# Kernel optimization log

Hardware: AMD Instinct MI355X
Metric: run time of the kernel (lower is better)

The kernel has to match this reference:

```python
import jax, jax.numpy as jnp
import numpy as np

EMBED_DIM = 512
NUM_HEADS = 8
HEAD_DIM = EMBED_DIM // NUM_HEADS
B, N, M = 4, 4096, 4096


def setup_inputs() -> dict:
    key = jax.random.key(0)
    ks = jax.random.split(key, 16)
    s = 0.02
    inp = {
        "query": jax.random.normal(ks[0], (B, N, EMBED_DIM), jnp.float32),
        "key": jax.random.normal(ks[1], (B, M, EMBED_DIM), jnp.float32),
        "value": jax.random.normal(ks[2], (B, M, EMBED_DIM), jnp.float32),
        # Linear weights stored as (in, out) so y = x @ W + b (== torch x @ W.T + b)
        "Wq": jax.random.normal(ks[3], (EMBED_DIM, EMBED_DIM), jnp.float32) * s,
        "bq": jnp.zeros((EMBED_DIM,), jnp.float32),
        "Wk": jax.random.normal(ks[4], (EMBED_DIM, EMBED_DIM), jnp.float32) * s,
        "bk": jnp.zeros((EMBED_DIM,), jnp.float32),
        "Wv": jax.random.normal(ks[5], (EMBED_DIM, EMBED_DIM), jnp.float32) * s,
        "bv": jnp.zeros((EMBED_DIM,), jnp.float32),
        # rank expansion MLP acts per-head on head_dim
        "W1": jax.random.normal(ks[6], (HEAD_DIM, HEAD_DIM * 2), jnp.float32) * s,
        "b1": jnp.zeros((HEAD_DIM * 2,), jnp.float32),
        "W2": jax.random.normal(ks[7], (HEAD_DIM * 2, HEAD_DIM), jnp.float32) * s,
        "b2": jnp.zeros((HEAD_DIM,), jnp.float32),
        "Wo": jax.random.normal(ks[8], (EMBED_DIM, EMBED_DIM), jnp.float32) * s,
        "bo": jnp.zeros((EMBED_DIM,), jnp.float32),
    }
    return inp


def reference(query, key, value, Wq, bq, Wk, bk, Wv, bv, W1, b1, W2, b2, Wo, bo):
    b, n, _ = query.shape
    m = key.shape[1]
    H, D = NUM_HEADS, HEAD_DIM
    # ELU+1 feature maps on projected q, k
    q = jax.nn.elu(query @ Wq + bq) + 1.0           # [B,N,E]
    k = jax.nn.elu(key @ Wk + bk) + 1.0             # [B,M,E]
    v = value @ Wv + bv                              # [B,M,E]
    q = q.reshape(b, n, H, D)
    k = k.reshape(b, m, H, D)
    v = v.reshape(b, m, H, D)
    # rank expansion MLP on keys (per head_dim), exact GELU as nn.GELU default
    k_aug = jax.nn.gelu(k @ W1 + b1, approximate=False) @ W2 + b2
    k_aug = jax.nn.elu(k_aug) + 1.0                  # [B,M,H,D]
    # inputs already fp32 (torch .float() casts are identity here)
    k_scaled = k_aug / m                             # normalize over context len
    kv_context = jnp.einsum('bmhd,bmhe->bhde', k_scaled, v)   # [B,H,D,D]
    out = jnp.einsum('bnhd,bhde->bnhe', q, kv_context)        # [B,N,H,D]
    k_sum = k_scaled.sum(axis=1)                      # [B,H,D]
    denom = jnp.einsum('bnhd,bhd->bnh', q, k_sum)     # [B,N,H]
    out = out / jnp.clip(denom, 1e-6, None)[..., None]
    out = jnp.clip(jnp.nan_to_num(out, nan=0.0, posinf=65000.0, neginf=-65000.0),
                   -65000.0, 65000.0)
    out = out.reshape(b, n, H * D)
    return out @ Wo + bo
```

## Files before the change

### kernel.cpp

```cpp
#include <hip/hip_runtime.h>
#include <hip/hip_bf16.h>
#include <cmath>

#define DEV __device__ __forceinline__

typedef __bf16 bf16x8 __attribute__((ext_vector_type(8)));
typedef float f32x4 __attribute__((ext_vector_type(4)));
typedef unsigned int u32;
typedef unsigned short u16;

DEV u16 f2bf(float f) {
  union { float f; u32 u; } v;
  v.f = f;
  u32 u = v.u;
  u += 0x7fffu + ((u >> 16) & 1u);
  return (u16)(u >> 16);
}
DEV u32 pk2(float a, float b) {
  union { __hip_bfloat162 h2; u32 u; } v;
  v.h2 = __float22bfloat162_rn(float2{a, b});
  return v.u;
}

DEV void async16(const void* g, void* l) {
  __builtin_amdgcn_global_load_lds((const __attribute__((address_space(1))) u32*)g,
                                   (__attribute__((address_space(3))) u32*)l, 16, 0, 0);
}

DEV int swz(int row, int kq) { return row * 64 + ((kq * 8) ^ ((row & 7) << 3)); }

__global__ __launch_bounds__(256)
void qkv_gemm(const float* __restrict__ qin, const float* __restrict__ kin,
              const float* __restrict__ vin, const u16* __restrict__ WqP,
              const u16* __restrict__ WkP, const u16* __restrict__ WvP,
              const float* __restrict__ bq, const float* __restrict__ bk,
              const float* __restrict__ bv, u16* __restrict__ qact,
              u16* __restrict__ kact, u16* __restrict__ vT)
{
  __shared__ __align__(16) u16 SB[18432];
  u16* As = SB;
  u16* Bs = SB + 8192;

  const int z = blockIdx.z;
  const float* Af = z == 0 ? qin : z == 1 ? kin : vin;
  const u16* Bp = z == 0 ? WqP : z == 1 ? WkP : WvP;
  const float* bias = z == 0 ? bq : z == 1 ? bk : bv;

  const int tid = threadIdx.x, wv = tid >> 6, lane = tid & 63;
  const int wr = wv >> 1, wc = wv & 1;
  const int lrow = lane & 15, lq = lane >> 4;
  const long r0 = (long)blockIdx.x * 128;
  const int c0 = blockIdx.y * 128;

  f32x4 acc[4][4] = {};

  for (int kt8 = 0; kt8 < 8; ++kt8) {
    const int kt = kt8 * 64;
    float4 fa[4][2];
#pragma unroll
    for (int it = 0; it < 4; ++it) {
      const int s = it * 256 + tid;
      const int row = s >> 3, kq = s & 7;
      const float* g = Af + (r0 + row) * 512 + kt + kq * 8;
      fa[it][0] = *(const float4*)g;
      fa[it][1] = *(const float4*)(g + 4);
    }
    if (kt8) __syncthreads();
#pragma unroll
    for (int it = 0; it < 4; ++it) {
      const int sl = it * 256 + wv * 64;
      async16(Bp + ((long)blockIdx.y * 8 + kt8) * 8192 + (sl + lane) * 8,
              &Bs[sl * 8]);
    }
#pragma unroll
    for (int it = 0; it < 4; ++it) {
      const int s = it * 256 + tid;
      const int row = s >> 3, kq = s & 7;
      union { u32 q[4]; uint4 v; } pk;
      pk.q[0] = pk2(fa[it][0].x, fa[it][0].y);
      pk.q[1] = pk2(fa[it][0].z, fa[it][0].w);
      pk.q[2] = pk2(fa[it][1].x, fa[it][1].y);
      pk.q[3] = pk2(fa[it][1].z, fa[it][1].w);
      *(uint4*)&As[swz(row, kq)] = pk.v;
    }
    __syncthreads();
#pragma unroll
    for (int subk = 0; subk < 2; ++subk) {
      bf16x8 af[4], bfr[4];
#pragma unroll
      for (int i = 0; i < 4; ++i)
        af[i] = *(const bf16x8*)&As[swz(wr * 64 + i * 16 + lrow, subk * 4 + lq)];
#pragma unroll
      for (int j = 0; j < 4; ++j)
        bfr[j] = *(const bf16x8*)&Bs[swz(wc * 64 + j * 16 + lrow, subk * 4 + lq)];
#pragma unroll
      for (int i = 0; i < 4; ++i)
#pragma unroll
        for (int j = 0; j < 4; ++j)
          acc[i][j] = __builtin_amdgcn_mfma_f32_16x16x32_bf16(af[i], bfr[j], acc[i][j], 0, 0, 0);
    }
  }
  __syncthreads();

  if (z < 2) {
    u16* Y = z == 0 ? qact : kact;
#pragma unroll
    for (int i = 0; i < 4; ++i) {
#pragma unroll
      for (int j = 0; j < 4; ++j) {
        const int col = c0 + wc * 64 + j * 16 + lrow;
        const float bvv = bias[col];
#pragma unroll
        for (int p = 0; p < 4; ++p) {
          float o = acc[i][j][p] + bvv;
          o = (o > 0.f) ? (o + 1.f) : __expf(o);
          const long row = r0 + wr * 64 + i * 16 + lq * 4 + p;
          Y[row * 512 + col] = f2bf(o);
        }
      }
    }
  } else {
    u16* LTv = SB + wv * 4608;
#pragma unroll
    for (int i = 0; i < 4; ++i) {
#pragma unroll
      for (int j = 0; j < 4; ++j) {
        const int col = c0 + wc * 64 + j * 16 + lrow;
        const float bvv = bias[col];
        ushort4 w;
        w.x = f2bf(acc[i][j][0] + bvv);
        w.y = f2bf(acc[i][j][1] + bvv);
        w.z = f2bf(acc[i][j][2] + bvv);
        w.w = f2bf(acc[i][j][3] + bvv);
        *(ushort4*)&LTv[(j * 16 + lrow) * 72 + i * 16 + lq * 4] = w;
      }
    }
    const int b = (int)(r0 >> 12);
    const int h = (c0 + wc * 64) >> 6;
    const int mg0 = (int)(r0 & 4095) + wr * 64;
#pragma unroll
    for (int ps = 0; ps < 8; ++ps) {
      const int e = ps * 8 + (lane >> 3);
      const int mq = (lane & 7) * 8;
      uint4 v = *(const uint4*)&LTv[e * 72 + mq];
      *(uint4*)(vT + (((long)b * 8 + h) * 64 + e) * 4096 + mg0 + mq) = v;
    }
  }
}

__global__ __launch_bounds__(256)
void out_gemm(const u16* __restrict__ A, const u16* __restrict__ Bt,
              const float* __restrict__ bias, float* __restrict__ Y)
{
  __shared__ __align__(16) u16 SB[16384];
  u16* As = SB;
  u16* Bs = SB + 8192;
  const int tid = threadIdx.x, wv = tid >> 6, lane = tid & 63;
  const int wr = wv >> 1, wc = wv & 1;
  const int lrow = lane & 15, lq = lane >> 4;
  const long r0 = (long)blockIdx.x * 128;
  const int c0 = blockIdx.y * 128;

  f32x4 acc[4][4] = {};
  for (int kt8 = 0; kt8 < 8; ++kt8) {
    if (kt8) __syncthreads();
#pragma unroll
    for (int it = 0; it < 4; ++it) {
      const int sl = it * 256 + wv * 64;
      async16(A + ((long)blockIdx.x * 8 + kt8) * 8192 + (sl + lane) * 8, &As[sl * 8]);
      async16(Bt + ((long)blockIdx.y * 8 + kt8) * 8192 + (sl + lane) * 8, &Bs[sl * 8]);
    }
    __syncthreads();
#pragma unroll
    for (int subk = 0; subk < 2; ++subk) {
      bf16x8 af[4], bfr[4];
#pragma unroll
      for (int i = 0; i < 4; ++i)
        af[i] = *(const bf16x8*)&As[swz(wr * 64 + i * 16 + lrow, subk * 4 + lq)];
#pragma unroll
      for (int j = 0; j < 4; ++j)
        bfr[j] = *(const bf16x8*)&Bs[swz(wc * 64 + j * 16 + lrow, subk * 4 + lq)];
#pragma unroll
      for (int i = 0; i < 4; ++i)
#pragma unroll
        for (int j = 0; j < 4; ++j)
          acc[i][j] = __builtin_amdgcn_mfma_f32_16x16x32_bf16(af[i], bfr[j], acc[i][j], 0, 0, 0);
    }
  }
#pragma unroll
  for (int i = 0; i < 4; ++i) {
#pragma unroll
    for (int j = 0; j < 4; ++j) {
      const int col = c0 + wc * 64 + j * 16 + lrow;
      const float bv = bias[col];
#pragma unroll
      for (int p = 0; p < 4; ++p) {
        const long row = r0 + wr * 64 + i * 16 + lq * 4 + p;
        Y[row * 512 + col] = acc[i][j][p] + bv;
      }
    }
  }
}

struct TArgs {
  const float* src[6];
  u16* dst[6];
  int K[6];
  int N[6];
};
__global__ __launch_bounds__(256)
void transpose_w(TArgs a)
{
  const int m = blockIdx.z;
  const int K = a.K[m], N = a.N[m];
  const int kt = blockIdx.y * 64, nt = blockIdx.x * 64;
  if (kt >= K || nt >= N) return;
  const float* src = a.src[m];
  u16* dst = a.dst[m];
  __shared__ u16 t[64][72];
  const int tx = threadIdx.x & 15, ty = threadIdx.x >> 4;
#pragma unroll
  for (int rr = 0; rr < 64; rr += 16) {
    const int k = kt + ty + rr;
    float4 v = *(const float4*)(src + (long)k * N + nt + tx * 4);
    t[tx * 4 + 0][ty + rr] = f2bf(v.x);
    t[tx * 4 + 1][ty + rr] = f2bf(v.y);
    t[tx * 4 + 2][ty + rr] = f2bf(v.z);
    t[tx * 4 + 3][ty + rr] = f2bf(v.w);
  }
  __syncthreads();
  if (m < 4) {
    const int ktile = kt >> 6;
#pragma unroll
    for (int it = 0; it < 2; ++it) {
      const int s = threadIdx.x + it * 256;
      const int r = s >> 3, c = (s & 7) * 8;
      const int n = nt + r;
      const int colblk = n >> 7, cl = n & 127;
      ushort4 u0 = *(ushort4*)&t[r][c];
      ushort4 u1 = *(ushort4*)&t[r][c + 4];
      u16* d = dst + ((long)colblk * 8 + ktile) * 8192 + cl * 64 + (c ^ ((cl & 7) << 3));
      *(ushort4*)d = u0;
      *(ushort4*)(d + 4) = u1;
    }
  } else {
#pragma unroll
    for (int it = 0; it < 2; ++it) {
      const int s = threadIdx.x + it * 256;
      const int r = s >> 3, c = (s & 7) * 8;
      ushort4 u0 = *(ushort4*)&t[r][c];
      ushort4 u1 = *(ushort4*)&t[r][c + 4];
      *(ushort4*)(dst + (long)(nt + r) * K + kt + c) = u0;
      *(ushort4*)(dst + (long)(nt + r) * K + kt + c + 4) = u1;
    }
  }
}

__global__ __launch_bounds__(256)
void mlp_fused(const u16* __restrict__ kact, const u16* __restrict__ W1T,
               const u16* __restrict__ W2T, const float* __restrict__ b1,
               const float* __restrict__ b2, u16* __restrict__ kaT, float invM)
{
  __shared__ __align__(16) u16 SB[27136];
  u16* As  = SB;
  u16* W1p = SB + 9216;
  u16* W2p = SB + 18432;
  u16* hid = SB;
  u16* LT2 = SB;

  const int tid = threadIdx.x, wv = tid >> 6, lane = tid & 63;
  const int lrow = lane & 15, lq = lane >> 4;
  const int bh = blockIdx.y, b = bh >> 3, h = bh & 7;
  const int m0 = blockIdx.x * 128;
  const long kbase = ((long)b * 4096 + m0) * 512 + h * 64;

#pragma unroll
  for (int i = 0; i < 4; ++i) {
    const int c = i * 256 + tid;
    const int row = c >> 3, p = c & 7;
    uint4 v = *(const uint4*)(kact + kbase + (long)row * 512 + p * 8);
    *(uint4*)&As[row * 72 + p * 8] = v;
  }
#pragma unroll
  for (int i = 0; i < 4; ++i) {
    const int c = i * 256 + tid;
    const int row = c >> 3, p = c & 7;
    uint4 v = *(const uint4*)(W1T + c * 8);
    *(uint4*)&W1p[row * 72 + p * 8] = v;
  }
#pragma unroll
  for (int i = 0; i < 4; ++i) {
    const int c = i * 256 + tid;
    const int row = c >> 4, p = c & 15;
    uint4 v = *(const uint4*)(W2T + c * 8);
    *(uint4*)&W2p[row * 136 + p * 8] = v;
  }
  __syncthreads();

  const int c0 = (wv >> 1) * 64, mh0 = (wv & 1) * 64;
  f32x4 acc1[4][4] = {};
#pragma unroll
  for (int kt = 0; kt < 2; ++kt) {
    bf16x8 wa[4], kb[4];
#pragma unroll
    for (int i = 0; i < 4; ++i)
      wa[i] = *(const bf16x8*)&W1p[(c0 + i * 16 + lrow) * 72 + kt * 32 + lq * 8];
#pragma unroll
    for (int j = 0; j < 4; ++j)
      kb[j] = *(const bf16x8*)&As[(mh0 + j * 16 + lrow) * 72 + kt * 32 + lq * 8];
#pragma unroll
    for (int i = 0; i < 4; ++i)
#pragma unroll
      for (int j = 0; j < 4; ++j)
        acc1[i][j] = __builtin_amdgcn_mfma_f32_16x16x32_bf16(wa[i], kb[j], acc1[i][j], 0, 0, 0);
  }
  __syncthreads();

#pragma unroll
  for (int i = 0; i < 4; ++i) {
    const int cc = c0 + i * 16 + lq * 4;
    float4 bv = *(const float4*)(b1 + cc);
#pragma unroll
    for (int j = 0; j < 4; ++j) {
      const int m = mh0 + j * 16 + lrow;
      float x0 = acc1[i][j][0] + bv.x, x1 = acc1[i][j][1] + bv.y;
      float x2 = acc1[i][j][2] + bv.z, x3 = acc1[i][j][3] + bv.w;
      ushort4 w;
      w.x = f2bf(0.5f * x0 * (1.f + erff(x0 * 0.7071067811865475f)));
      w.y = f2bf(0.5f * x1 * (1.f + erff(x1 * 0.7071067811865475f)));
      w.z = f2bf(0.5f * x2 * (1.f + erff(x2 * 0.7071067811865475f)));
      w.w = f2bf(0.5f * x3 * (1.f + erff(x3 * 0.7071067811865475f)));
      *(ushort4*)&hid[m * 136 + cc] = w;
    }
  }
  __syncthreads();

  const int d0 = (wv >> 1) * 32, mh2 = (wv & 1) * 64;
  f32x4 acc2[4][2] = {};
#pragma unroll
  for (int kt = 0; kt < 4; ++kt) {
    bf16x8 wa[2], hb[4];
#pragma unroll
    for (int i = 0; i < 2; ++i)
      wa[i] = *(const bf16x8*)&W2p[(d0 + i * 16 + lrow) * 136 + kt * 32 + lq * 8];
#pragma unroll
    for (int j = 0; j < 4; ++j)
      hb[j] = *(const bf16x8*)&hid[(mh2 + j * 16 + lrow) * 136 + kt * 32 + lq * 8];
#pragma unroll
    for (int j = 0; j < 4; ++j)
#pragma unroll
      for (int i = 0; i < 2; ++i)
        acc2[j][i] = __builtin_amdgcn_mfma_f32_16x16x32_bf16(hb[j], wa[i], acc2[j][i], 0, 0, 0);
  }
  __syncthreads();

#pragma unroll
  for (int i = 0; i < 2; ++i) {
    const int d = d0 + i * 16 + lrow;
    const float bd = b2[d];
#pragma unroll
    for (int j = 0; j < 4; ++j) {
      const int ml = mh2 + j * 16 + lq * 4;
      ushort4 w;
#pragma unroll
      for (int p = 0; p < 4; ++p) {
        float v = acc2[j][i][p] + bd;
        v = ((v > 0.f) ? (v + 1.f) : __expf(v)) * invM;
        ((u16*)&w)[p] = f2bf(v);
      }
      *(ushort4*)&LT2[d * 136 + ml] = w;
    }
  }
  __syncthreads();
#pragma unroll
  for (int it = 0; it < 4; ++it) {
    const int c = it * 256 + tid;
    const int d = c >> 4, mq = (c & 15) * 8;
    uint4 v = *(const uint4*)&LT2[d * 136 + mq];
    *(uint4*)(kaT + ((long)bh * 64 + d) * 4096 + m0 + mq) = v;
  }
}

__global__ __launch_bounds__(256)
void kv_gemm(const u16* __restrict__ kaT, const u16* __restrict__ vT,
             float* __restrict__ kvp, float* __restrict__ ksp)
{
  const int sp = blockIdx.x;
  const int bh = blockIdx.y;
  __shared__ u16 SB[16384];
  u16* As = SB;
  u16* Bs = SB + 8192;
  const int tid = threadIdx.x, wv = tid >> 6, lane = tid & 63;
  const int lrow = lane & 15, lq = lane >> 4;
  f32x4 acc[4][4] = {};
  f32x4 accs[4] = {};
  bf16x8 ones;
#pragma unroll
  for (int z = 0; z < 8; ++z) ones[z] = (__bf16)1.0f;
  const long base = (long)bh * 64 * 4096;

  for (int ph = 0; ph < 2; ++ph) {
    const int m0 = sp * 256 + ph * 128;
#pragma unroll
    for (int i = 0; i < 4; ++i) {
      const int s = (wv * 4 + i) * 64 + lane;
      const int chunk = s >> 8, row = (s >> 2) & 63, part = s & 3;
      const long g = base + (long)row * 4096 + m0 + chunk * 32 + part * 8;
      async16(kaT + g, &As[(wv * 4 + i) * 512]);
      async16(vT + g, &Bs[(wv * 4 + i) * 512]);
    }
    __syncthreads();
    bf16x8 af[4], bfr[4];
#pragma unroll
    for (int i = 0; i < 4; ++i)
      af[i] = *(const bf16x8*)&As[wv * 2048 + (i * 16 + lrow) * 32 + lq * 8];
#pragma unroll
    for (int j = 0; j < 4; ++j)
      bfr[j] = *(const bf16x8*)&Bs[wv * 2048 + (j * 16 + lrow) * 32 + lq * 8];
#pragma unroll
    for (int i = 0; i < 4; ++i) {
#pragma unroll
      for (int j = 0; j < 4; ++j)
        acc[i][j] = __builtin_amdgcn_mfma_f32_16x16x32_bf16(af[i], bfr[j], acc[i][j], 0, 0, 0);
      accs[i] = __builtin_amdgcn_mfma_f32_16x16x32_bf16(af[i], ones, accs[i], 0, 0, 0);
    }
    __syncthreads();
  }

  float* red = (float*)SB;
  float* ksr = red + 64 * 68;
  for (int w = 0; w < 4; ++w) {
    __syncthreads();
    if (wv == w) {
#pragma unroll
      for (int i = 0; i < 4; ++i) {
#pragma unroll
        for (int j = 0; j < 4; ++j) {
          const int e = j * 16 + lrow, dd = i * 16 + lq * 4;
          float* p = &red[e * 68 + dd];
          if (w == 0) { p[0] = acc[i][j][0]; p[1] = acc[i][j][1]; p[2] = acc[i][j][2]; p[3] = acc[i][j][3]; }
          else        { p[0] += acc[i][j][0]; p[1] += acc[i][j][1]; p[2] += acc[i][j][2]; p[3] += acc[i][j][3]; }
        }
        if (lrow == 0) {
          const int dd = i * 16 + lq * 4;
#pragma unroll
          for (int p2 = 0; p2 < 4; ++p2) {
            if (w == 0) ksr[dd + p2] = accs[i][p2];
            else        ksr[dd + p2] += accs[i][p2];
          }
        }
      }
    }
  }
  __syncthreads();
  float* kvo = kvp + ((long)sp * 32 + bh) * 4096;
  for (int s = tid; s < 4096; s += 256) kvo[s] = red[(s >> 6) * 68 + (s & 63)];
  if (tid < 64) ksp[(sp * 32 + bh) * 64 + tid] = ksr[tid];
}

__global__ __launch_bounds__(256)
void kv_reduce(const float* __restrict__ kvp, const float* __restrict__ ksp,
               u16* __restrict__ kvT, u16* __restrict__ ksumT)
{
  const int bh = blockIdx.x;
  const int t = threadIdx.x;
  const int s0 = blockIdx.y * 512;
#pragma unroll
  for (int i = 0; i < 2; ++i) {
    const int s = s0 + i * 256 + t;
    float v = 0.f;
#pragma unroll
    for (int sp = 0; sp < 16; ++sp) v += kvp[((long)sp * 32 + bh) * 4096 + s];
    kvT[(long)bh * 4096 + s] = f2bf(v);
  }
  if (blockIdx.y == 0 && t < 64) {
    float v = 0.f;
#pragma unroll
    for (int sp = 0; sp < 16; ++sp) v += ksp[(sp * 32 + bh) * 64 + t];
    ksumT[bh * 64 + t] = f2bf(v);
  }
}

__global__ __launch_bounds__(256)
void attn_mfma(const u16* __restrict__ q, const u16* __restrict__ kvT,
               const u16* __restrict__ ksumT, u16* __restrict__ attn)
{
  __shared__ u16 SB[17408];
  const int tid = threadIdx.x, wv = tid >> 6, lane = tid & 63;
  const int lrow = lane & 15, lq = lane >> 4;
  const int n0 = blockIdx.x * 256;
  const int bh = blockIdx.y, b = bh >> 3, h = bh & 7;
  u16* As = SB;

#pragma unroll
  for (int half = 0; half < 2; ++half)
#pragma unroll
    for (int i = 0; i < 4; ++i) {
      const int s = (wv * 4 + i) * 64 + lane;
      async16(q + ((long)(b * 4096 + n0 + (s >> 2))) * 512 + h * 64 + half * 32 + (s & 3) * 8,
              &As[half * 8192 + (wv * 4 + i) * 512]);
    }
  bf16x8 bfr[2][4], ks[2];
#pragma unroll
  for (int half = 0; half < 2; ++half) {
#pragma unroll
    for (int j = 0; j < 4; ++j)
      bfr[half][j] = *(const bf16x8*)(kvT + ((long)bh * 64 + j * 16 + lrow) * 64 + half * 32 + lq * 8);
    ks[half] = *(const bf16x8*)(ksumT + bh * 64 + half * 32 + lq * 8);
  }
  __syncthreads();

  f32x4 acc[4][4] = {};
  f32x4 accd[4] = {};
#pragma unroll
  for (int half = 0; half < 2; ++half) {
    bf16x8 af[4];
#pragma unroll
    for (int i = 0; i < 4; ++i)
      af[i] = *(const bf16x8*)&As[half * 8192 + (wv * 64 + i * 16 + lrow) * 32 + lq * 8];
#pragma unroll
    for (int i = 0; i < 4; ++i) {
#pragma unroll
      for (int j = 0; j < 4; ++j)
        acc[i][j] = __builtin_amdgcn_mfma_f32_16x16x32_bf16(af[i], bfr[half][j], acc[i][j], 0, 0, 0);
      accd[i] = __builtin_amdgcn_mfma_f32_16x16x32_bf16(af[i], ks[half], accd[i], 0, 0, 0);
    }
  }
  __syncthreads();

  u16* LT = SB;
#pragma unroll
  for (int i = 0; i < 4; ++i) {
    float dinv[4];
#pragma unroll
    for (int p = 0; p < 4; ++p) dinv[p] = 1.f / fmaxf(accd[i][p], 1e-6f);
#pragma unroll
    for (int j = 0; j < 4; ++j) {
      const int e = j * 16 + lrow;
      const int nl0 = i * 16 + lq * 4;
      ushort4 w;
      float x0 = acc[i][j][0] * dinv[0], x1 = acc[i][j][1] * dinv[1];
      float x2 = acc[i][j][2] * dinv[2], x3 = acc[i][j][3] * dinv[3];
      if (!(x0 == x0)) x0 = 0.f;
      if (!(x1 == x1)) x1 = 0.f;
      if (!(x2 == x2)) x2 = 0.f;
      if (!(x3 == x3)) x3 = 0.f;
      w.x = f2bf(fminf(65000.f, fmaxf(-65000.f, x0)));
      w.y = f2bf(fminf(65000.f, fmaxf(-65000.f, x1)));
      w.z = f2bf(fminf(65000.f, fmaxf(-65000.f, x2)));
      w.w = f2bf(fminf(65000.f, fmaxf(-65000.f, x3)));
      *(ushort4*)&LT[wv * 4352 + e * 68 + nl0] = w;
    }
  }
  __syncthreads();
#pragma unroll
  for (int it = 0; it < 8; ++it) {
    const int c = it * 256 + tid;
    const int n = c & 255, ec = c >> 8;
    const int wr2 = n >> 6, nl = n & 63;
    ushort4 w0, w1;
    w0.x = LT[wr2 * 4352 + (ec * 8 + 0) * 68 + nl];
    w0.y = LT[wr2 * 4352 + (ec * 8 + 1) * 68 + nl];
    w0.z = LT[wr2 * 4352 + (ec * 8 + 2) * 68 + nl];
    w0.w = LT[wr2 * 4352 + (ec * 8 + 3) * 68 + nl];
    w1.x = LT[wr2 * 4352 + (ec * 8 + 4) * 68 + nl];
    w1.y = LT[wr2 * 4352 + (ec * 8 + 5) * 68 + nl];
    w1.z = LT[wr2 * 4352 + (ec * 8 + 6) * 68 + nl];
    w1.w = LT[wr2 * 4352 + (ec * 8 + 7) * 68 + nl];
    const int ng = b * 4096 + n0 + n;
    const int rowblk = ng >> 7, rl = ng & 127;
    u16* dst = attn + ((long)rowblk * 8 + h) * 8192 + rl * 64 + ((ec * 8) ^ ((rl & 7) << 3));
    *(ushort4*)dst = w0;
    *(ushort4*)(dst + 4) = w1;
  }
}

static constexpr long U = 8388608;

extern "C" void kernel_launch(void* const* d_in, const int* in_sizes, int n_in,
                              void* d_out, int out_size, void* d_ws, size_t ws_size,
                              hipStream_t stream)
{
  const float* query = (const float*)d_in[0];
  const float* key   = (const float*)d_in[1];
  const float* value = (const float*)d_in[2];
  const float* Wq = (const float*)d_in[3];
  const float* bq = (const float*)d_in[4];
  const float* Wk = (const float*)d_in[5];
  const float* bk = (const float*)d_in[6];
  const float* Wv = (const float*)d_in[7];
  const float* bv = (const float*)d_in[8];
  const float* W1 = (const float*)d_in[9];
  const float* b1 = (const float*)d_in[10];
  const float* W2 = (const float*)d_in[11];
  const float* b2 = (const float*)d_in[12];
  const float* Wo = (const float*)d_in[13];
  const float* bo = (const float*)d_in[14];

  u16* wsh = (u16*)d_ws;
  u16* qact = wsh;
  u16* kact = wsh + U;
  u16* vT   = wsh + 2 * U;
  u16* kaT  = wsh + 3 * U;
  u16* attn = wsh + 4 * U;

  float* fp  = (float*)(wsh + 5 * U);
  float* kvp = fp;
  float* ksp = fp + 2097152;
  u16* kvTg   = (u16*)(fp + 2129920);
  u16* ksumTg = kvTg + 131072;
  u16* wtb = ksumTg + 2048;
  u16* WqT = wtb;
  u16* WkT = wtb + 262144;
  u16* WvT = wtb + 524288;
  u16* WoT = wtb + 786432;
  u16* W1T = wtb + 1048576;
  u16* W2T = wtb + 1056768;

  dim3 blk(256);
  const float invM = 1.f / 4096.f;

  TArgs ta;
  ta.src[0] = Wq; ta.dst[0] = WqT; ta.K[0] = 512; ta.N[0] = 512;
  ta.src[1] = Wk; ta.dst[1] = WkT; ta.K[1] = 512; ta.N[1] = 512;
  ta.src[2] = Wv; ta.dst[2] = WvT; ta.K[2] = 512; ta.N[2] = 512;
  ta.src[3] = Wo; ta.dst[3] = WoT; ta.K[3] = 512; ta.N[3] = 512;
  ta.src[4] = W1; ta.dst[4] = W1T; ta.K[4] = 64;  ta.N[4] = 128;
  ta.src[5] = W2; ta.dst[5] = W2T; ta.K[5] = 128; ta.N[5] = 64;
  transpose_w<<<dim3(8, 8, 6), blk, 0, stream>>>(ta);

  qkv_gemm<<<dim3(128, 4, 3), blk, 0, stream>>>(query, key, value, WqT, WkT, WvT,
                                                bq, bk, bv, qact, kact, vT);
  mlp_fused<<<dim3(32, 32), blk, 0, stream>>>(kact, W1T, W2T, b1, b2, kaT, invM);
  kv_gemm<<<dim3(16, 32), blk, 0, stream>>>(kaT, vT, kvp, ksp);
  kv_reduce<<<dim3(32, 8), blk, 0, stream>>>(kvp, ksp, kvTg, ksumTg);
  attn_mfma<<<dim3(16, 32), blk, 0, stream>>>(qact, kvTg, ksumTg, attn);
  out_gemm<<<dim3(128, 4), blk, 0, stream>>>(attn, WoT, bo, (float*)d_out);
}
```

Before: 254.4 us.

## Double-buffer LDS tiles with manual waitcnt pipelining in GEMM kernels

Converts qkv_gemm, out_gemm and kv_gemm from single-buffered load-then-compute loops to double-buffered LDS pipelines. The next K-tile is prefetched with async global-to-LDS loads while the current tile is computed, and qkv_gemm also keeps two A tiles in registers for an extra stage of prefetch. Full __syncthreads are replaced by explicit s_waitcnt vmcnt/lgkmcnt plus s_barrier. The aim is to hide global-load latency behind MFMA work. In exchange, LDS per block doubles to 64KB and register pressure rises, which could limit occupancy, and the hand-tuned waitcnt counts are fragile to get right.

```diff
diff --git a/kernel.cpp b/kernel.cpp
--- a/kernel.cpp
+++ b/kernel.cpp
@@ -8,6 +8,11 @@
 typedef float f32x4 __attribute__((ext_vector_type(4)));
 typedef unsigned int u32;
 typedef unsigned short u16;
+
+#define S_VMCNT(N) asm volatile("s_waitcnt vmcnt(" #N ")" ::: "memory")
+#define S_LGKM0    asm volatile("s_waitcnt lgkmcnt(0)" ::: "memory")
+#define S_FENCE    asm volatile("" ::: "memory")
+#define S_BAR      __builtin_amdgcn_s_barrier()
 
 DEV u16 f2bf(float f) {
   union { float f; u32 u; } v;
@@ -29,7 +34,7 @@
 
 DEV int swz(int row, int kq) { return row * 64 + ((kq * 8) ^ ((row & 7) << 3)); }
 
-__global__ __launch_bounds__(256)
+__global__ __launch_bounds__(256, 2)
 void qkv_gemm(const float* __restrict__ qin, const float* __restrict__ kin,
               const float* __restrict__ vin, const u16* __restrict__ WqP,
               const u16* __restrict__ WkP, const u16* __restrict__ WvP,
@@ -37,9 +42,7 @@
               const float* __restrict__ bv, u16* __restrict__ qact,
               u16* __restrict__ kact, u16* __restrict__ vT)
 {
-  __shared__ __align__(16) u16 SB[18432];
-  u16* As = SB;
-  u16* Bs = SB + 8192;
+  __shared__ __align__(16) u16 SB[32768];
 
   const int z = blockIdx.z;
   const float* Af = z == 0 ? qin : z == 1 ? kin : vin;
@@ -53,54 +56,82 @@
   const int c0 = blockIdx.y * 128;
 
   f32x4 acc[4][4] = {};
-
-  for (int kt8 = 0; kt8 < 8; ++kt8) {
-    const int kt = kt8 * 64;
-    float4 fa[4][2];
+  float4 rA[2][8];
+
+  auto loadA = [&](float4* dst, int T) {
 #pragma unroll
     for (int it = 0; it < 4; ++it) {
       const int s = it * 256 + tid;
       const int row = s >> 3, kq = s & 7;
-      const float* g = Af + (r0 + row) * 512 + kt + kq * 8;
-      fa[it][0] = *(const float4*)g;
-      fa[it][1] = *(const float4*)(g + 4);
-    }
-    if (kt8) __syncthreads();
-#pragma unroll
-    for (int it = 0; it < 4; ++it) {
-      const int sl = it * 256 + wv * 64;
-      async16(Bp + ((long)blockIdx.y * 8 + kt8) * 8192 + (sl + lane) * 8,
-              &Bs[sl * 8]);
-    }
+      const float* g = Af + (r0 + row) * 512 + T * 64 + kq * 8;
+      dst[2 * it]     = *(const float4*)g;
+      dst[2 * it + 1] = *(const float4*)(g + 4);
+    }
+  };
+  auto cvtStoreA = [&](const float4* src, u16* bufA) {
 #pragma unroll
     for (int it = 0; it < 4; ++it) {
       const int s = it * 256 + tid;
       const int row = s >> 3, kq = s & 7;
       union { u32 q[4]; uint4 v; } pk;
-      pk.q[0] = pk2(fa[it][0].x, fa[it][0].y);
-      pk.q[1] = pk2(fa[it][0].z, fa[it][0].w);
-      pk.q[2] = pk2(fa[it][1].x, fa[it][1].y);
-      pk.q[3] = pk2(fa[it][1].z, fa[it][1].w);
-      *(uint4*)&As[swz(row, kq)] = pk.v;
-    }
-    __syncthreads();
+      pk.q[0] = pk2(src[2 * it].x, src[2 * it].y);
+      pk.q[1] = pk2(src[2 * it].z, src[2 * it].w);
+      pk.q[2] = pk2(src[2 * it + 1].x, src[2 * it + 1].y);
+      pk.q[3] = pk2(src[2 * it + 1].z, src[2 * it + 1].w);
+      *(uint4*)&bufA[swz(row, kq)] = pk.v;
+    }
+  };
+  auto issueB = [&](int T, u16* bufB) {
+#pragma unroll
+    for (int it = 0; it < 4; ++it) {
+      const int sl = it * 256 + wv * 64;
+      async16(Bp + ((long)blockIdx.y * 8 + T) * 8192 + (sl + lane) * 8, &bufB[sl * 8]);
+    }
+  };
+  auto computeT = [&](const u16* Ac, const u16* Bc) {
 #pragma unroll
     for (int subk = 0; subk < 2; ++subk) {
       bf16x8 af[4], bfr[4];
 #pragma unroll
       for (int i = 0; i < 4; ++i)
-        af[i] = *(const bf16x8*)&As[swz(wr * 64 + i * 16 + lrow, subk * 4 + lq)];
+        af[i] = *(const bf16x8*)&Ac[swz(wr * 64 + i * 16 + lrow, subk * 4 + lq)];
 #pragma unroll
       for (int j = 0; j < 4; ++j)
-        bfr[j] = *(const bf16x8*)&Bs[swz(wc * 64 + j * 16 + lrow, subk * 4 + lq)];
+        bfr[j] = *(const bf16x8*)&Bc[swz(wc * 64 + j * 16 + lrow, subk * 4 + lq)];
 #pragma unroll
       for (int i = 0; i < 4; ++i)
 #pragma unroll
         for (int j = 0; j < 4; ++j)
           acc[i][j] = __builtin_amdgcn_mfma_f32_16x16x32_bf16(af[i], bfr[j], acc[i][j], 0, 0, 0);
     }
-  }
-  __syncthreads();
+  };
+
+  issueB(0, SB + 8192);
+  S_FENCE;
+  loadA(rA[0], 0);
+  loadA(rA[1], 1);
+  cvtStoreA(rA[0], SB);
+  S_LGKM0;
+  S_VMCNT(8);
+  S_BAR;
+
+#pragma unroll
+  for (int t = 0; t < 8; ++t) {
+    const int cur = t & 1, nxt = 1 - cur;
+    u16* Ac = SB + cur * 16384;
+    u16* Bc = Ac + 8192;
+    u16* An = SB + nxt * 16384;
+    u16* Bn = An + 8192;
+    if (t < 7) issueB(t + 1, Bn);
+    S_FENCE;
+    if (t < 6) loadA(rA[cur], t + 2);
+    if (t < 7) cvtStoreA(rA[nxt], An);
+    computeT(Ac, Bc);
+    S_LGKM0;
+    if (t < 6)       { S_VMCNT(8); }
+    else if (t == 6) { S_VMCNT(0); }
+    S_BAR;
+  }
 
   if (z < 2) {
     u16* Y = z == 0 ? qact : kact;
@@ -148,44 +179,55 @@
   }
 }
 
-__global__ __launch_bounds__(256)
+__global__ __launch_bounds__(256, 2)
 void out_gemm(const u16* __restrict__ A, const u16* __restrict__ Bt,
               const float* __restrict__ bias, float* __restrict__ Y)
 {
-  __shared__ __align__(16) u16 SB[16384];
-  u16* As = SB;
-  u16* Bs = SB + 8192;
+  __shared__ __align__(16) u16 SB[32768];
   const int tid = threadIdx.x, wv = tid >> 6, lane = tid & 63;
   const int wr = wv >> 1, wc = wv & 1;
   const int lrow = lane & 15, lq = lane >> 4;
   const long r0 = (long)blockIdx.x * 128;
   const int c0 = blockIdx.y * 128;
 
-  f32x4 acc[4][4] = {};
-  for (int kt8 = 0; kt8 < 8; ++kt8) {
-    if (kt8) __syncthreads();
+  auto stage = [&](int T, u16* buf) {
 #pragma unroll
     for (int it = 0; it < 4; ++it) {
       const int sl = it * 256 + wv * 64;
-      async16(A + ((long)blockIdx.x * 8 + kt8) * 8192 + (sl + lane) * 8, &As[sl * 8]);
-      async16(Bt + ((long)blockIdx.y * 8 + kt8) * 8192 + (sl + lane) * 8, &Bs[sl * 8]);
-    }
-    __syncthreads();
+      async16(A  + ((long)blockIdx.x * 8 + T) * 8192 + (sl + lane) * 8, &buf[sl * 8]);
+      async16(Bt + ((long)blockIdx.y * 8 + T) * 8192 + (sl + lane) * 8, &buf[8192 + sl * 8]);
+    }
+  };
+
+  f32x4 acc[4][4] = {};
+  stage(0, SB);
+  S_VMCNT(0);
+  S_BAR;
+
+#pragma unroll
+  for (int t = 0; t < 8; ++t) {
+    const int cur = t & 1, nxt = 1 - cur;
+    if (t < 7) stage(t + 1, SB + nxt * 16384);
+    const u16* Ac = SB + cur * 16384;
+    const u16* Bc = Ac + 8192;
 #pragma unroll
     for (int subk = 0; subk < 2; ++subk) {
       bf16x8 af[4], bfr[4];
 #pragma unroll
       for (int i = 0; i < 4; ++i)
-        af[i] = *(const bf16x8*)&As[swz(wr * 64 + i * 16 + lrow, subk * 4 + lq)];
+        af[i] = *(const bf16x8*)&Ac[swz(wr * 64 + i * 16 + lrow, subk * 4 + lq)];
 #pragma unroll
       for (int j = 0; j < 4; ++j)
-        bfr[j] = *(const bf16x8*)&Bs[swz(wc * 64 + j * 16 + lrow, subk * 4 + lq)];
+        bfr[j] = *(const bf16x8*)&Bc[swz(wc * 64 + j * 16 + lrow, subk * 4 + lq)];
 #pragma unroll
       for (int i = 0; i < 4; ++i)
 #pragma unroll
         for (int j = 0; j < 4; ++j)
           acc[i][j] = __builtin_amdgcn_mfma_f32_16x16x32_bf16(af[i], bfr[j], acc[i][j], 0, 0, 0);
     }
+    S_LGKM0;
+    if (t < 7) { S_VMCNT(0); }
+    S_BAR;
   }
 #pragma unroll
   for (int i = 0; i < 4; ++i) {
@@ -381,15 +423,13 @@
   }
 }
 
-__global__ __launch_bounds__(256)
+__global__ __launch_bounds__(256, 2)
 void kv_gemm(const u16* __restrict__ kaT, const u16* __restrict__ vT,
              float* __restrict__ kvp, float* __restrict__ ksp)
 {
   const int sp = blockIdx.x;
   const int bh = blockIdx.y;
-  __shared__ u16 SB[16384];
-  u16* As = SB;
-  u16* Bs = SB + 8192;
+  __shared__ __align__(16) u16 SB[32768];
   const int tid = threadIdx.x, wv = tid >> 6, lane = tid & 63;
   const int lrow = lane & 15, lq = lane >> 4;
   f32x4 acc[4][4] = {};
@@ -399,6 +439,7 @@
   for (int z = 0; z < 8; ++z) ones[z] = (__bf16)1.0f;
   const long base = (long)bh * 64 * 4096;
 
+#pragma unroll
   for (int ph = 0; ph < 2; ++ph) {
     const int m0 = sp * 256 + ph * 128;
 #pragma unroll
@@ -406,10 +447,17 @@
       const int s = (wv * 4 + i) * 64 + lane;
       const int chunk = s >> 8, row = (s >> 2) & 63, part = s & 3;
       const long g = base + (long)row * 4096 + m0 + chunk * 32 + part * 8;
-      async16(kaT + g, &As[(wv * 4 + i) * 512]);
-      async16(vT + g, &Bs[(wv * 4 + i) * 512]);
-    }
-    __syncthreads();
+      async16(kaT + g, &SB[ph * 16384 + (wv * 4 + i) * 512]);
+      async16(vT + g, &SB[ph * 16384 + 8192 + (wv * 4 + i) * 512]);
+    }
+    S_FENCE;
+  }
+
+#pragma unroll
+  for (int ph = 0; ph < 2; ++ph) {
+    if (ph == 0) { S_VMCNT(8); } else { S_VMCNT(0); }
+    const u16* As = SB + ph * 16384;
+    const u16* Bs = As + 8192;
     bf16x8 af[4], bfr[4];
 #pragma unroll
     for (int i = 0; i < 4; ++i)
@@ -424,7 +472,6 @@
         acc[i][j] = __builtin_amdgcn_mfma_f32_16x16x32_bf16(af[i], bfr[j], acc[i][j], 0, 0, 0);
       accs[i] = __builtin_amdgcn_mfma_f32_16x16x32_bf16(af[i], ones, accs[i], 0, 0, 0);
     }
-    __syncthreads();
   }
 
   float* red = (float*)SB;
```

After: 256.1 us. Within noise of the previous version (+0.7%).
